# Performance work log

Measured on AMD Instinct MI355X. Metric: run time of the kernel, lower is better.

The kernel has to match this reference:

```python
import jax, jax.numpy as jnp
import numpy as np

N_X, N_UNITS, N_Y, N_U = 64, 256, 32, 64
BATCH = 32768


def setup_inputs() -> dict:
    key = jax.random.key(0)
    ks = jax.random.split(key, 10)
    nz = 2 * N_X + N_UNITS
    return {
        "u": jax.random.normal(ks[0], (BATCH, N_U, 1), dtype=jnp.float32),
        "x0": jax.random.normal(ks[1], (BATCH, N_X, 1), dtype=jnp.float32),
        # learned parameters (scaled down so H stays well-conditioned and tanh unsaturated)
        "B_2": 0.1 * jax.random.normal(ks[2], (N_X, N_U), dtype=jnp.float32),
        "C_2": 0.1 * jax.random.normal(ks[3], (N_Y, N_X), dtype=jnp.float32),
        "D_12": 0.1 * jax.random.normal(ks[4], (N_UNITS, N_U), dtype=jnp.float32),
        "D_21": 0.1 * jax.random.normal(ks[5], (N_Y, N_UNITS), dtype=jnp.float32),
        "b": 0.1 * jax.random.normal(ks[6], (N_X + N_UNITS + N_Y, 1), dtype=jnp.float32),
        "X": (1.0 / np.sqrt(nz)) * jax.random.normal(ks[7], (nz, nz), dtype=jnp.float32),
        "Y1": 0.1 * jax.random.normal(ks[8], (N_X, N_X), dtype=jnp.float32),
        # fixed IQC multipliers (train_qsr=False): Q nsd, R=I so Rinv=I; S stored transposed
        "S_t": 0.1 * jax.random.normal(ks[9], (N_U, N_Y), dtype=jnp.float32),
        "Q": -jnp.eye(N_Y, dtype=jnp.float32),
        "Rinv": jnp.eye(N_U, dtype=jnp.float32),
    }


def _constrained_weights(B_2, C_2, D_12, D_21, X, S_t, Q, Rinv):
    """Port of REN.updateConstrainedWeights (train_qsr=False). Returns C_1, D_11, lam."""
    n_x, n_units = B_2.shape[0], D_12.shape[0]
    n_y = C_2.shape[0]
    nz = 2 * n_x + n_units
    C2_ = S_t @ C_2                       # [n_u, n_x]
    D21_ = S_t @ D_21 - D_12.T            # [n_u, n_units]
    H = X.T @ X + 1e-3 * jnp.eye(nz, dtype=X.dtype)
    lT1 = jnp.concatenate([C2_.T, D21_.T, B_2], axis=0)          # [nz, n_u]
    H = H + lT1 @ Rinv @ lT1.T
    lT2 = jnp.concatenate([C_2.T, D_21.T, jnp.zeros((n_x, n_y), dtype=X.dtype)], axis=0)
    H = H - lT2 @ Q @ lT2.T
    H_21 = H[n_x:n_x + n_units, :n_x]
    H_22 = H[n_x:n_x + n_units, n_x:n_x + n_units]
    C_1 = -H_21                           # [n_units, n_x]
    lam = 0.5 * jnp.diag(H_22)            # Lambda diagonal, > 0 since H is PD
    # L = tril(-(H_22 - diag(H_22))) == -strictly_lower(H_22)
    D_11 = -jnp.tril(H_22, k=-1)          # strictly lower triangular [n_units, n_units]
    return C_1, D_11, lam


def _forward(u, x0, B_2, C_2, D_12, D_21, b, X, Y1, S_t, Q, Rinv):
    n_x, n_units = B_2.shape[0], D_12.shape[0]
    C_1, D_11, lam = _constrained_weights(B_2, C_2, D_12, D_21, X, S_t, Q, Rinv)
    u2 = u[:, :, 0]                       # [B, n_u]
    x2 = x0[:, :, 0]                      # [B, n_x]
    b_w = b[n_x:n_x + n_units, 0]         # [n_units]
    b_y = b[n_x + n_units:, 0]            # [n_y]
    # precompute the non-recurrent part of the pre-activation for all units
    v = x2 @ C_1.T + u2 @ D_12.T + b_w    # [B, n_units]
    # NOTE: the source uses D_11 row (i_unit - 1), not i_unit (faithful to original code).
    # For i=0 the source uses term2 = 0; D_11 is strictly lower so the full-row dot
    # against the partially-filled w (zeros beyond index i) matches D_11[i-1, :i] @ w[:i].
    Drows = jnp.concatenate([jnp.zeros((1, n_units), dtype=D_11.dtype), D_11[:-1]], axis=0)
    batch = u2.shape[0]

    def step(w, i):
        wi = jnp.tanh((v[:, i] + w @ Drows[i]) / lam[i])   # [B]
        w = w.at[:, i].set(wi)
        return w, None

    w0 = jnp.zeros((batch, n_units), dtype=v.dtype)
    w, _ = jax.lax.scan(step, w0, jnp.arange(n_units))
    y = x2 @ C_2.T + w @ D_21.T + b_y     # [B, n_y]
    return y[:, :, None]                  # [B, n_y, 1]


def reference(u, x0, B_2, C_2, D_12, D_21, b, X, Y1, S_t, Q, Rinv):
    return _forward(u, x0, B_2, C_2, D_12, D_21, b, X, Y1, S_t, Q, Rinv)
```

## Files before the change

### kernel.cpp

```cpp
#include <hip/hip_runtime.h>
#include <hip/hip_bf16.h>

typedef __attribute__((ext_vector_type(8))) short short8;
typedef __attribute__((ext_vector_type(4))) float floatx4;
typedef __attribute__((ext_vector_type(2))) float floatx2;

#define MFMA16 __builtin_amdgcn_mfma_f32_16x16x32_bf16

__device__ inline unsigned short bf16_rn(float f) {
    return (unsigned short)((__float_as_uint(f) + 0x8000u) >> 16);
}
__device__ __attribute__((always_inline)) inline short8 pack8v(float4 a, float4 b) {
    union { short8 s; unsigned int u[4]; } r;
    union { __hip_bfloat162 h; unsigned int u; } c;
    c.h = __float22bfloat162_rn(make_float2(a.x, a.y)); r.u[0] = c.u;
    c.h = __float22bfloat162_rn(make_float2(a.z, a.w)); r.u[1] = c.u;
    c.h = __float22bfloat162_rn(make_float2(b.x, b.y)); r.u[2] = c.u;
    c.h = __float22bfloat162_rn(make_float2(b.z, b.w)); r.u[3] = c.u;
    return r.s;
}

__global__ __launch_bounds__(64) void ren_prep13(
    const float* __restrict__ B2, const float* __restrict__ C2,
    const float* __restrict__ D12, const float* __restrict__ D21,
    const float* __restrict__ St, const float* __restrict__ Q,
    const float* __restrict__ Rinv,
    float* __restrict__ lT1, float* __restrict__ t1,
    float* __restrict__ lT2, float* __restrict__ t2,
    unsigned short* __restrict__ Wvb, unsigned short* __restrict__ C2b,
    unsigned short* __restrict__ D21b)
{
    const int t = threadIdx.x;
    const int blk = blockIdx.x;
    if (blk >= 384) {
        const int id = (blk - 384) * 64 + t;
        if (id < 16384) {
            Wvb[(id >> 6) * 128 + 64 + (id & 63)] = bf16_rn(D12[id]);
        } else if (id < 16384 + 2048) {
            C2b[id - 16384] = bf16_rn(C2[id - 16384]);
        } else if (id < 16384 + 2048 + 8192) {
            D21b[id - 18432] = bf16_rn(D21[id - 18432]);
        }
        return;
    }

    __shared__ float stl[64 * 33];
    __shared__ float colbuf[32];
    __shared__ float s1[64];

    const int r = blk;
    const int c = t;
#pragma unroll
    for (int j = 0; j < 32; j++) {
        const int id = j * 64 + t;
        stl[(id >> 5) * 33 + (id & 31)] = St[id];
    }
    if (t < 32)
        colbuf[t] = (r < 64) ? C2[t * 64 + r]
                  : (r < 320 ? D21[t * 256 + (r - 64)] : 0.f);
    __syncthreads();

    float v1;
    if (r < 64) {
        float s = 0.f;
#pragma unroll
        for (int p = 0; p < 32; p++) s += stl[c * 33 + p] * colbuf[p];
        v1 = s;
    } else if (r < 320) {
        float s = 0.f;
#pragma unroll
        for (int p = 0; p < 32; p++) s += stl[c * 33 + p] * colbuf[p];
        v1 = s - D12[(r - 64) * 64 + c];
    } else {
        v1 = B2[(r - 320) * 64 + c];
    }
    s1[c] = v1;
    lT1[r * 64 + c] = v1;
    if (c < 32) {
        const float v2 = (r < 320) ? colbuf[c] : 0.f;
        lT2[r * 32 + c] = v2;
    }
    __syncthreads();

    float a = 0.f;
#pragma unroll
    for (int k = 0; k < 64; k++) a += s1[k] * Rinv[k * 64 + c];
    t1[r * 64 + c] = a;

    if (c < 32) {
        float bq = 0.f;
#pragma unroll
        for (int k = 0; k < 32; k++) bq += colbuf[k] * Q[k * 32 + c];
        t2[r * 32 + c] = bq;
    }
}

__global__ __launch_bounds__(320) void ren_prep2(
    const float* __restrict__ X,
    const float* __restrict__ lT1, const float* __restrict__ t1,
    const float* __restrict__ lT2, const float* __restrict__ t2,
    unsigned short* __restrict__ Wvb, unsigned short* __restrict__ Drowsb,
    float* __restrict__ Dpair, float* __restrict__ lamg)
{
    __shared__ float xcol[384];
    const int c = threadIdx.x;
    const int i = blockIdx.x;
    for (int t = c; t < 384; t += 320) xcol[t] = X[t * 384 + 64 + i];
    __syncthreads();

    float f0 = 0.f, f1 = 0.f, f2 = 0.f, f3 = 0.f;
    float ac[8], au[8], bc8[8], bu[8];
#pragma unroll
    for (int kk = 0; kk < 8; kk++) { ac[kk] = X[kk * 384 + c]; au[kk] = xcol[kk]; }
    for (int k0 = 0; k0 < 384; k0 += 16) {
#pragma unroll
        for (int kk = 0; kk < 8; kk++) {
            bc8[kk] = X[(k0 + 8 + kk) * 384 + c]; bu[kk] = xcol[k0 + 8 + kk];
        }
        f0 += au[0] * ac[0]; f1 += au[1] * ac[1];
        f2 += au[2] * ac[2]; f3 += au[3] * ac[3];
        f0 += au[4] * ac[4]; f1 += au[5] * ac[5];
        f2 += au[6] * ac[6]; f3 += au[7] * ac[7];
        if (k0 + 16 < 384) {
#pragma unroll
            for (int kk = 0; kk < 8; kk++) {
                ac[kk] = X[(k0 + 16 + kk) * 384 + c]; au[kk] = xcol[k0 + 16 + kk];
            }
        }
        f0 += bu[0] * bc8[0]; f1 += bu[1] * bc8[1];
        f2 += bu[2] * bc8[2]; f3 += bu[3] * bc8[3];
        f0 += bu[4] * bc8[4]; f1 += bu[5] * bc8[5];
        f2 += bu[6] * bc8[6]; f3 += bu[7] * bc8[7];
    }

    const float* __restrict__ t1r = t1 + (64 + i) * 64;
    const float* __restrict__ l1r = lT1 + c * 64;
#pragma unroll
    for (int m4 = 0; m4 < 16; m4++) {
        const float4 lv = *(const float4*)(l1r + m4 * 4);
        f0 += t1r[m4 * 4 + 0] * lv.x; f1 += t1r[m4 * 4 + 1] * lv.y;
        f2 += t1r[m4 * 4 + 2] * lv.z; f3 += t1r[m4 * 4 + 3] * lv.w;
    }
    const float* __restrict__ t2r = t2 + (64 + i) * 32;
    const float* __restrict__ l2r = lT2 + c * 32;
#pragma unroll
    for (int m4 = 0; m4 < 8; m4++) {
        const float4 lv = *(const float4*)(l2r + m4 * 4);
        f0 -= t2r[m4 * 4 + 0] * lv.x; f1 -= t2r[m4 * 4 + 1] * lv.y;
        f2 -= t2r[m4 * 4 + 2] * lv.z; f3 -= t2r[m4 * 4 + 3] * lv.w;
    }
    float acc = (f0 + f1) + (f2 + f3) + (((64 + i) == c) ? 0.001f : 0.f);

    if (c < 64) {
        Wvb[i * 128 + c] = bf16_rn(-acc);
    } else {
        const int cb = c - 64;
        if (cb == i) lamg[i] = 5.7707801635558536f / acc;
        if (i < 255) {
            const float dv = (cb <= i - 1) ? -acc : 0.f;
            Drowsb[(i + 1) * 256 + cb] = bf16_rn(dv);
            const int row = i + 1;
            if ((row >> 4) == (cb >> 4)) {
                const int q = row & 15, p = cb & 15;
                Dpair[(row >> 4) * 256 + (q >> 1) * 32 + p * 2 + (q & 1)] = dv;
            }
        } else {
            Drowsb[cb] = 0;
        }
    }
}

__device__ __attribute__((always_inline)) inline void triangle16x2(
    float (&vlA)[16], float (&wlA)[16],
    float (&vlB)[16], float (&wlB)[16],
    const float* __restrict__ dblk, const float* __restrict__ lam)
{
#pragma unroll
    for (int tq = 0; tq < 8; tq++) {
        floatx2 aA, bA, aB, bB;
        aA[0] = vlA[2 * tq]; aA[1] = vlA[2 * tq + 1];
        aB[0] = vlB[2 * tq]; aB[1] = vlB[2 * tq + 1];
        bA[0] = 0.f; bA[1] = 0.f;
        bB[0] = 0.f; bB[1] = 0.f;
#pragma unroll
        for (int p4 = 0; p4 < tq; p4++) {
            const float4 d4 = *(const float4*)&dblk[tq * 32 + p4 * 4];
            floatx2 de; de[0] = d4.x; de[1] = d4.y;
            floatx2 dz; dz[0] = d4.z; dz[1] = d4.w;
            aA += de * wlA[2 * p4];  bA += dz * wlA[2 * p4 + 1];
            aB += de * wlB[2 * p4];  bB += dz * wlB[2 * p4 + 1];
        }
        aA += bA; aB += bB;
        floatx2 lm2; lm2[0] = lam[2 * tq]; lm2[1] = lam[2 * tq + 1];
        aA *= lm2; aB *= lm2;
        const float e0A = __builtin_amdgcn_exp2f(aA[0]);
        const float e1A = __builtin_amdgcn_exp2f(aA[1]);
        const float e0B = __builtin_amdgcn_exp2f(aB[0]);
        const float e1B = __builtin_amdgcn_exp2f(aB[1]);
        wlA[2 * tq]     = 1.f - 2.f * __builtin_amdgcn_rcpf(e0A + 1.f);
        wlA[2 * tq + 1] = 1.f - 2.f * __builtin_amdgcn_rcpf(e1A + 1.f);
        wlB[2 * tq]     = 1.f - 2.f * __builtin_amdgcn_rcpf(e0B + 1.f);
        wlB[2 * tq + 1] = 1.f - 2.f * __builtin_amdgcn_rcpf(e1B + 1.f);
    }
}

__global__ __launch_bounds__(64, 1) void ren_main(
    const float* __restrict__ u, const float* __restrict__ x0,
    const float* __restrict__ b,
    const unsigned short* __restrict__ Wvb,
    const unsigned short* __restrict__ Drowsb,
    const float* __restrict__ Dpair,
    const float* __restrict__ lamg,
    const unsigned short* __restrict__ C2b,
    const unsigned short* __restrict__ D21b,
    float* __restrict__ out)
{
    __shared__ float bufA[16][20];
    __shared__ float bufB[16][20];
    __shared__ float dblk[256];
    __shared__ float lamsh[256];
    __shared__ float bsh[256];
    __shared__ short8 wshA[8 * 64];
    __shared__ short8 wshB[8 * 64];

    const int L = threadIdx.x;
    const int col = L & 15;
    const int quad = L >> 4;
    const int row0 = blockIdx.x * 32;

#pragma unroll
    for (int j = 0; j < 4; j++) {
        lamsh[j * 64 + L] = lamg[j * 64 + L];
        bsh[j * 64 + L]   = b[64 + j * 64 + L];
    }
    const short8 zero8 = {0, 0, 0, 0, 0, 0, 0, 0};
#pragma unroll
    for (int c = 0; c < 8; c++) { wshA[c * 64 + L] = zero8; wshB[c * 64 + L] = zero8; }

    short8 zfA[4], zfB[4];
#pragma unroll
    for (int c = 0; c < 4; c++) {
        const float* base = (c < 2 ? x0 : u);
        const float* pA = base + (long)(row0 + col) * 64 + (c & 1) * 32 + quad * 8;
        const float* pB = base + (long)(row0 + 16 + col) * 64 + (c & 1) * 32 + quad * 8;
        zfA[c] = pack8v(*(const float4*)pA, *(const float4*)(pA + 4));
        zfB[c] = pack8v(*(const float4*)pB, *(const float4*)(pB + 4));
    }

    float4 dcur = *(const float4*)(Dpair + 4 * L);
    floatx4 accA0 = {0.f, 0.f, 0.f, 0.f}, accA1 = {0.f, 0.f, 0.f, 0.f};
    floatx4 accB0 = {0.f, 0.f, 0.f, 0.f}, accB1 = {0.f, 0.f, 0.f, 0.f};
    {
        short8 v0 = *(const short8*)(Wvb + col * 128 + quad * 8);
        short8 v1 = *(const short8*)(Wvb + col * 128 + 32 + quad * 8);
        short8 v2 = *(const short8*)(Wvb + col * 128 + 64 + quad * 8);
        short8 v3 = *(const short8*)(Wvb + col * 128 + 96 + quad * 8);
        accA0 = MFMA16(zfA[0], v0, accA0, 0, 0, 0);
        accB0 = MFMA16(zfB[0], v0, accB0, 0, 0, 0);
        accA1 = MFMA16(zfA[1], v1, accA1, 0, 0, 0);
        accB1 = MFMA16(zfB[1], v1, accB1, 0, 0, 0);
        accA0 = MFMA16(zfA[2], v2, accA0, 0, 0, 0);
        accB0 = MFMA16(zfB[2], v2, accB0, 0, 0, 0);
        accA1 = MFMA16(zfA[3], v3, accA1, 0, 0, 0);
        accB1 = MFMA16(zfB[3], v3, accB1, 0, 0, 0);
    }

#pragma unroll 1
    for (int n = 0; n < 15; n++) {
        const int rb = 16 * (n + 1) + col;
        float4 dnxt = *(const float4*)(Dpair + (n + 1) * 256 + 4 * L);
        short8 vf[4];
#pragma unroll
        for (int c = 0; c < 4; c++)
            vf[c] = *(const short8*)(Wvb + rb * 128 + c * 32 + quad * 8);

        *(float4*)&dblk[4 * L] = dcur;
        const float bwv = bsh[16 * n + col];
#pragma unroll
        for (int r = 0; r < 4; r++) {
            bufA[quad * 4 + r][col] = accA0[r] + accA1[r] + bwv;
            bufB[quad * 4 + r][col] = accB0[r] + accB1[r] + bwv;
        }

        float vlA[16], wlA[16], vlB[16], wlB[16];
#pragma unroll
        for (int p4 = 0; p4 < 4; p4++) {
            const float4 ta = *(const float4*)&bufA[col][p4 * 4];
            const float4 tb = *(const float4*)&bufB[col][p4 * 4];
            vlA[p4 * 4 + 0] = ta.x; vlA[p4 * 4 + 1] = ta.y;
            vlA[p4 * 4 + 2] = ta.z; vlA[p4 * 4 + 3] = ta.w;
            vlB[p4 * 4 + 0] = tb.x; vlB[p4 * 4 + 1] = tb.y;
            vlB[p4 * 4 + 2] = tb.z; vlB[p4 * 4 + 3] = tb.w;
        }

        triangle16x2(vlA, wlA, vlB, wlB, dblk, &lamsh[16 * n]);

        {
            float4 waA, wbA, waB, wbB;
            if (quad & 1) {
                waA = make_float4(wlA[8], wlA[9], wlA[10], wlA[11]);
                wbA = make_float4(wlA[12], wlA[13], wlA[14], wlA[15]);
                waB = make_float4(wlB[8], wlB[9], wlB[10], wlB[11]);
                wbB = make_float4(wlB[12], wlB[13], wlB[14], wlB[15]);
            } else {
                waA = make_float4(wlA[0], wlA[1], wlA[2], wlA[3]);
                wbA = make_float4(wlA[4], wlA[5], wlA[6], wlA[7]);
                waB = make_float4(wlB[0], wlB[1], wlB[2], wlB[3]);
                wbB = make_float4(wlB[4], wlB[5], wlB[6], wlB[7]);
            }
            const short8 nfA = pack8v(waA, wbA);
            const short8 nfB = pack8v(waB, wbB);
            if ((quad >> 1) == (n & 1)) {
                wshA[(n >> 1) * 64 + L] = nfA;
                wshB[(n >> 1) * 64 + L] = nfB;
            }
        }

        floatx4 aA0 = {0.f, 0.f, 0.f, 0.f}, aA1 = {0.f, 0.f, 0.f, 0.f};
        floatx4 aB0 = {0.f, 0.f, 0.f, 0.f}, aB1 = {0.f, 0.f, 0.f, 0.f};
        aA0 = MFMA16(zfA[0], vf[0], aA0, 0, 0, 0);
        aB0 = MFMA16(zfB[0], vf[0], aB0, 0, 0, 0);
        aA1 = MFMA16(zfA[1], vf[1], aA1, 0, 0, 0);
        aB1 = MFMA16(zfB[1], vf[1], aB1, 0, 0, 0);
        aA0 = MFMA16(zfA[2], vf[2], aA0, 0, 0, 0);
        aB0 = MFMA16(zfB[2], vf[2], aB0, 0, 0, 0);
        aA1 = MFMA16(zfA[3], vf[3], aA1, 0, 0, 0);
        aB1 = MFMA16(zfB[3], vf[3], aB1, 0, 0, 0);
        const int lim = (n + 2) >> 1;
#pragma unroll 1
        for (int c = 0; c < lim; c++) {
            const short8 h = *(const short8*)(Drowsb + rb * 256 + c * 32 + quad * 8);
            const short8 wA = wshA[c * 64 + L];
            const short8 wB = wshB[c * 64 + L];
            if (c & 1) {
                aA1 = MFMA16(wA, h, aA1, 0, 0, 0);
                aB1 = MFMA16(wB, h, aB1, 0, 0, 0);
            } else {
                aA0 = MFMA16(wA, h, aA0, 0, 0, 0);
                aB0 = MFMA16(wB, h, aB0, 0, 0, 0);
            }
        }
        accA0 = aA0; accA1 = aA1; accB0 = aB0; accB1 = aB1;
        dcur = dnxt;
    }

    {
        *(float4*)&dblk[4 * L] = dcur;
        const float bwv = bsh[240 + col];
#pragma unroll
        for (int r = 0; r < 4; r++) {
            bufA[quad * 4 + r][col] = accA0[r] + accA1[r] + bwv;
            bufB[quad * 4 + r][col] = accB0[r] + accB1[r] + bwv;
        }

        float vlA[16], wlA[16], vlB[16], wlB[16];
#pragma unroll
        for (int p4 = 0; p4 < 4; p4++) {
            const float4 ta = *(const float4*)&bufA[col][p4 * 4];
            const float4 tb = *(const float4*)&bufB[col][p4 * 4];
            vlA[p4 * 4 + 0] = ta.x; vlA[p4 * 4 + 1] = ta.y;
            vlA[p4 * 4 + 2] = ta.z; vlA[p4 * 4 + 3] = ta.w;
            vlB[p4 * 4 + 0] = tb.x; vlB[p4 * 4 + 1] = tb.y;
            vlB[p4 * 4 + 2] = tb.z; vlB[p4 * 4 + 3] = tb.w;
        }

        triangle16x2(vlA, wlA, vlB, wlB, dblk, &lamsh[240]);

        float4 waA, wbA, waB, wbB;
        if (quad & 1) {
            waA = make_float4(wlA[8], wlA[9], wlA[10], wlA[11]);
            wbA = make_float4(wlA[12], wlA[13], wlA[14], wlA[15]);
            waB = make_float4(wlB[8], wlB[9], wlB[10], wlB[11]);
            wbB = make_float4(wlB[12], wlB[13], wlB[14], wlB[15]);
        } else {
            waA = make_float4(wlA[0], wlA[1], wlA[2], wlA[3]);
            wbA = make_float4(wlA[4], wlA[5], wlA[6], wlA[7]);
            waB = make_float4(wlB[0], wlB[1], wlB[2], wlB[3]);
            wbB = make_float4(wlB[4], wlB[5], wlB[6], wlB[7]);
        }
        const short8 nfA = pack8v(waA, wbA);
        const short8 nfB = pack8v(waB, wbB);
        if (quad >= 2) {
            wshA[7 * 64 + L] = nfA;
            wshB[7 * 64 + L] = nfB;
        }
    }

    floatx4 yA0 = {0.f, 0.f, 0.f, 0.f}, yA1 = {0.f, 0.f, 0.f, 0.f};
    floatx4 yB0 = {0.f, 0.f, 0.f, 0.f}, yB1 = {0.f, 0.f, 0.f, 0.f};
    {
        const short8 yc0 = *(const short8*)(C2b + col * 64 + quad * 8);
        const short8 yc1 = *(const short8*)(C2b + col * 64 + 32 + quad * 8);
        const short8 yc2 = *(const short8*)(C2b + (16 + col) * 64 + quad * 8);
        const short8 yc3 = *(const short8*)(C2b + (16 + col) * 64 + 32 + quad * 8);
        yA0 = MFMA16(zfA[0], yc0, yA0, 0, 0, 0);
        yB0 = MFMA16(zfB[0], yc0, yB0, 0, 0, 0);
        yA1 = MFMA16(zfA[0], yc2, yA1, 0, 0, 0);
        yB1 = MFMA16(zfB[0], yc2, yB1, 0, 0, 0);
        yA0 = MFMA16(zfA[1], yc1, yA0, 0, 0, 0);
        yB0 = MFMA16(zfB[1], yc1, yB0, 0, 0, 0);
        yA1 = MFMA16(zfA[1], yc3, yA1, 0, 0, 0);
        yB1 = MFMA16(zfB[1], yc3, yB1, 0, 0, 0);
    }
#pragma unroll
    for (int c = 0; c < 8; c++) {
        const short8 wA = wshA[c * 64 + L];
        const short8 wB = wshB[c * 64 + L];
        const short8 b0 = *(const short8*)(D21b + col * 256 + c * 32 + quad * 8);
        const short8 b1 = *(const short8*)(D21b + (16 + col) * 256 + c * 32 + quad * 8);
        yA0 = MFMA16(wA, b0, yA0, 0, 0, 0);
        yB0 = MFMA16(wB, b0, yB0, 0, 0, 0);
        yA1 = MFMA16(wA, b1, yA1, 0, 0, 0);
        yB1 = MFMA16(wB, b1, yB1, 0, 0, 0);
    }
    const float by0 = b[320 + col];
    const float by1 = b[336 + col];
#pragma unroll
    for (int r = 0; r < 4; r++) {
        out[(long)(row0 + quad * 4 + r) * 32 + col]           = yA0[r] + by0;
        out[(long)(row0 + quad * 4 + r) * 32 + 16 + col]      = yA1[r] + by1;
        out[(long)(row0 + 16 + quad * 4 + r) * 32 + col]      = yB0[r] + by0;
        out[(long)(row0 + 16 + quad * 4 + r) * 32 + 16 + col] = yB1[r] + by1;
    }
}

extern "C" void kernel_launch(void* const* d_in, const int* in_sizes, int n_in,
                              void* d_out, int out_size, void* d_ws, size_t ws_size,
                              hipStream_t stream)
{
    const float* u    = (const float*)d_in[0];
    const float* x0   = (const float*)d_in[1];
    const float* B2   = (const float*)d_in[2];
    const float* C2   = (const float*)d_in[3];
    const float* D12  = (const float*)d_in[4];
    const float* D21  = (const float*)d_in[5];
    const float* b    = (const float*)d_in[6];
    const float* X    = (const float*)d_in[7];
    const float* St   = (const float*)d_in[9];
    const float* Q    = (const float*)d_in[10];
    const float* Rinv = (const float*)d_in[11];
    float* out = (float*)d_out;

    float* ws     = (float*)d_ws;
    float* lT1    = ws;
    float* t1     = lT1 + 384 * 64;
    float* lT2    = t1 + 384 * 64;
    float* t2     = lT2 + 384 * 32;
    float* lamg   = t2 + 384 * 32;
    float* Dpair  = lamg + 256;
    unsigned short* Drowsb = (unsigned short*)(Dpair + 16 * 256);
    unsigned short* Wvb    = Drowsb + 256 * 256;
    unsigned short* C2b    = Wvb + 256 * 128;
    unsigned short* D21b   = C2b + 32 * 64;

    ren_prep13<<<dim3(800), dim3(64), 0, stream>>>(B2, C2, D12, D21, St, Q, Rinv,
                                                   lT1, t1, lT2, t2, Wvb, C2b, D21b);
    ren_prep2<<<dim3(256), dim3(320), 0, stream>>>(X, lT1, t1, lT2, t2,
                                                   Wvb, Drowsb, Dpair, lamg);

    const int batch = in_sizes[0] / 64;
    ren_main<<<dim3(batch / 32), dim3(64), 0, stream>>>(u, x0, b, Wvb, Drowsb,
                                                        Dpair, lamg, C2b, D21b, out);
}
```

Measured before the change: 137.6 us.

## Prefetch next block's weights into double-buffered registers and fully unroll Drows loop

Restructures the 15-step recurrent block loop into unrolled pairs. Each step now preloads the Wvb and Drows fragments for the following block into register buffers that alternate between steps, so the global loads overlap the triangle solve and MFMAs. The inner Drows loop becomes a fixed, fully unrolled 8-chunk loop. This removes the loop control and the load-use stalls, but it always runs 8 chunks of MFMAs even where only a few are needed. It also raises register pressure and relies on the not-yet-written shared w chunks multiplying zero weights harmlessly.

```diff
diff --git a/kernel.cpp b/kernel.cpp
--- a/kernel.cpp
+++ b/kernel.cpp
@@ -204,6 +204,78 @@
     }
 }
 
+#define REN_ITER(n_, VC, HC, VN, HN, DO_LOAD_)                                 \
+  {                                                                            \
+    const int nI = (n_);                                                       \
+    if (DO_LOAD_) {                                                            \
+      const int rb2 = 16 * (nI + 2) + col;                                     \
+      _Pragma("unroll") for (int cc = 0; cc < 4; cc++)                         \
+        VN[cc] = *(const short8*)(Wvb + rb2 * 128 + cc * 32 + quad * 8);       \
+      _Pragma("unroll") for (int cc = 0; cc < 8; cc++)                         \
+        HN[cc] = *(const short8*)(Drowsb + rb2 * 256 + cc * 32 + quad * 8);    \
+    }                                                                          \
+    const float4 dnxtI = *(const float4*)(Dpair + (nI + 1) * 256 + 4 * L);     \
+    *(float4*)&dblk[4 * L] = dcur;                                             \
+    const float bwvI = bsh[16 * nI + col];                                     \
+    _Pragma("unroll") for (int r = 0; r < 4; r++) {                            \
+      bufA[quad * 4 + r][col] = accA0[r] + accA1[r] + bwvI;                    \
+      bufB[quad * 4 + r][col] = accB0[r] + accB1[r] + bwvI;                    \
+    }                                                                          \
+    float vlA[16], wlA[16], vlB[16], wlB[16];                                  \
+    _Pragma("unroll") for (int p4 = 0; p4 < 4; p4++) {                         \
+      const float4 ta = *(const float4*)&bufA[col][p4 * 4];                    \
+      const float4 tb = *(const float4*)&bufB[col][p4 * 4];                    \
+      vlA[p4 * 4 + 0] = ta.x; vlA[p4 * 4 + 1] = ta.y;                          \
+      vlA[p4 * 4 + 2] = ta.z; vlA[p4 * 4 + 3] = ta.w;                          \
+      vlB[p4 * 4 + 0] = tb.x; vlB[p4 * 4 + 1] = tb.y;                          \
+      vlB[p4 * 4 + 2] = tb.z; vlB[p4 * 4 + 3] = tb.w;                          \
+    }                                                                          \
+    triangle16x2(vlA, wlA, vlB, wlB, dblk, &lamsh[16 * nI]);                   \
+    {                                                                          \
+      float4 waA, wbA, waB, wbB;                                               \
+      if (quad & 1) {                                                          \
+        waA = make_float4(wlA[8], wlA[9], wlA[10], wlA[11]);                   \
+        wbA = make_float4(wlA[12], wlA[13], wlA[14], wlA[15]);                 \
+        waB = make_float4(wlB[8], wlB[9], wlB[10], wlB[11]);                   \
+        wbB = make_float4(wlB[12], wlB[13], wlB[14], wlB[15]);                 \
+      } else {                                                                 \
+        waA = make_float4(wlA[0], wlA[1], wlA[2], wlA[3]);                     \
+        wbA = make_float4(wlA[4], wlA[5], wlA[6], wlA[7]);                     \
+        waB = make_float4(wlB[0], wlB[1], wlB[2], wlB[3]);                     \
+        wbB = make_float4(wlB[4], wlB[5], wlB[6], wlB[7]);                     \
+      }                                                                        \
+      const short8 nfA = pack8v(waA, wbA);                                     \
+      const short8 nfB = pack8v(waB, wbB);                                     \
+      if ((quad >> 1) == (nI & 1)) {                                           \
+        wshA[(nI >> 1) * 64 + L] = nfA;                                        \
+        wshB[(nI >> 1) * 64 + L] = nfB;                                        \
+      }                                                                        \
+    }                                                                          \
+    floatx4 aA0 = {0.f, 0.f, 0.f, 0.f}, aA1 = {0.f, 0.f, 0.f, 0.f};            \
+    floatx4 aB0 = {0.f, 0.f, 0.f, 0.f}, aB1 = {0.f, 0.f, 0.f, 0.f};            \
+    aA0 = MFMA16(zfA[0], VC[0], aA0, 0, 0, 0);                                 \
+    aB0 = MFMA16(zfB[0], VC[0], aB0, 0, 0, 0);                                 \
+    aA1 = MFMA16(zfA[1], VC[1], aA1, 0, 0, 0);                                 \
+    aB1 = MFMA16(zfB[1], VC[1], aB1, 0, 0, 0);                                 \
+    aA0 = MFMA16(zfA[2], VC[2], aA0, 0, 0, 0);                                 \
+    aB0 = MFMA16(zfB[2], VC[2], aB0, 0, 0, 0);                                 \
+    aA1 = MFMA16(zfA[3], VC[3], aA1, 0, 0, 0);                                 \
+    aB1 = MFMA16(zfB[3], VC[3], aB1, 0, 0, 0);                                 \
+    _Pragma("unroll") for (int cc = 0; cc < 8; cc++) {                         \
+      const short8 wA = wshA[cc * 64 + L];                                     \
+      const short8 wB = wshB[cc * 64 + L];                                     \
+      if (cc & 1) {                                                            \
+        aA1 = MFMA16(wA, HC[cc], aA1, 0, 0, 0);                                \
+        aB1 = MFMA16(wB, HC[cc], aB1, 0, 0, 0);                                \
+      } else {                                                                 \
+        aA0 = MFMA16(wA, HC[cc], aA0, 0, 0, 0);                                \
+        aB0 = MFMA16(wB, HC[cc], aB0, 0, 0, 0);                                \
+      }                                                                        \
+    }                                                                          \
+    accA0 = aA0; accA1 = aA1; accB0 = aB0; accB1 = aB1;                        \
+    dcur = dnxtI;                                                              \
+  }
+
 __global__ __launch_bounds__(64, 1) void ren_main(
     const float* __restrict__ u, const float* __restrict__ x0,
     const float* __restrict__ b,
@@ -265,84 +337,23 @@
         accB1 = MFMA16(zfB[3], v3, accB1, 0, 0, 0);
     }
 
+    short8 sv0[4], sh0[8], sv1[4], sh1[8];
+    {
+        const int rb = 16 + col;
+#pragma unroll
+        for (int c = 0; c < 4; c++)
+            sv1[c] = *(const short8*)(Wvb + rb * 128 + c * 32 + quad * 8);
+#pragma unroll
+        for (int c = 0; c < 8; c++)
+            sh1[c] = *(const short8*)(Drowsb + rb * 256 + c * 32 + quad * 8);
+    }
+
 #pragma unroll 1
-    for (int n = 0; n < 15; n++) {
-        const int rb = 16 * (n + 1) + col;
-        float4 dnxt = *(const float4*)(Dpair + (n + 1) * 256 + 4 * L);
-        short8 vf[4];
-#pragma unroll
-        for (int c = 0; c < 4; c++)
-            vf[c] = *(const short8*)(Wvb + rb * 128 + c * 32 + quad * 8);
-
-        *(float4*)&dblk[4 * L] = dcur;
-        const float bwv = bsh[16 * n + col];
-#pragma unroll
-        for (int r = 0; r < 4; r++) {
-            bufA[quad * 4 + r][col] = accA0[r] + accA1[r] + bwv;
-            bufB[quad * 4 + r][col] = accB0[r] + accB1[r] + bwv;
-        }
-
-        float vlA[16], wlA[16], vlB[16], wlB[16];
-#pragma unroll
-        for (int p4 = 0; p4 < 4; p4++) {
-            const float4 ta = *(const float4*)&bufA[col][p4 * 4];
-            const float4 tb = *(const float4*)&bufB[col][p4 * 4];
-            vlA[p4 * 4 + 0] = ta.x; vlA[p4 * 4 + 1] = ta.y;
-            vlA[p4 * 4 + 2] = ta.z; vlA[p4 * 4 + 3] = ta.w;
-            vlB[p4 * 4 + 0] = tb.x; vlB[p4 * 4 + 1] = tb.y;
-            vlB[p4 * 4 + 2] = tb.z; vlB[p4 * 4 + 3] = tb.w;
-        }
-
-        triangle16x2(vlA, wlA, vlB, wlB, dblk, &lamsh[16 * n]);
-
-        {
-            float4 waA, wbA, waB, wbB;
-            if (quad & 1) {
-                waA = make_float4(wlA[8], wlA[9], wlA[10], wlA[11]);
-                wbA = make_float4(wlA[12], wlA[13], wlA[14], wlA[15]);
-                waB = make_float4(wlB[8], wlB[9], wlB[10], wlB[11]);
-                wbB = make_float4(wlB[12], wlB[13], wlB[14], wlB[15]);
-            } else {
-                waA = make_float4(wlA[0], wlA[1], wlA[2], wlA[3]);
-                wbA = make_float4(wlA[4], wlA[5], wlA[6], wlA[7]);
-                waB = make_float4(wlB[0], wlB[1], wlB[2], wlB[3]);
-                wbB = make_float4(wlB[4], wlB[5], wlB[6], wlB[7]);
-            }
-            const short8 nfA = pack8v(waA, wbA);
-            const short8 nfB = pack8v(waB, wbB);
-            if ((quad >> 1) == (n & 1)) {
-                wshA[(n >> 1) * 64 + L] = nfA;
-                wshB[(n >> 1) * 64 + L] = nfB;
-            }
-        }
-
-        floatx4 aA0 = {0.f, 0.f, 0.f, 0.f}, aA1 = {0.f, 0.f, 0.f, 0.f};
-        floatx4 aB0 = {0.f, 0.f, 0.f, 0.f}, aB1 = {0.f, 0.f, 0.f, 0.f};
-        aA0 = MFMA16(zfA[0], vf[0], aA0, 0, 0, 0);
-        aB0 = MFMA16(zfB[0], vf[0], aB0, 0, 0, 0);
-        aA1 = MFMA16(zfA[1], vf[1], aA1, 0, 0, 0);
-        aB1 = MFMA16(zfB[1], vf[1], aB1, 0, 0, 0);
-        aA0 = MFMA16(zfA[2], vf[2], aA0, 0, 0, 0);
-        aB0 = MFMA16(zfB[2], vf[2], aB0, 0, 0, 0);
-        aA1 = MFMA16(zfA[3], vf[3], aA1, 0, 0, 0);
-        aB1 = MFMA16(zfB[3], vf[3], aB1, 0, 0, 0);
-        const int lim = (n + 2) >> 1;
-#pragma unroll 1
-        for (int c = 0; c < lim; c++) {
-            const short8 h = *(const short8*)(Drowsb + rb * 256 + c * 32 + quad * 8);
-            const short8 wA = wshA[c * 64 + L];
-            const short8 wB = wshB[c * 64 + L];
-            if (c & 1) {
-                aA1 = MFMA16(wA, h, aA1, 0, 0, 0);
-                aB1 = MFMA16(wB, h, aB1, 0, 0, 0);
-            } else {
-                aA0 = MFMA16(wA, h, aA0, 0, 0, 0);
-                aB0 = MFMA16(wB, h, aB0, 0, 0, 0);
-            }
-        }
-        accA0 = aA0; accA1 = aA1; accB0 = aB0; accB1 = aB1;
-        dcur = dnxt;
-    }
+    for (int np = 0; np < 7; np++) {
+        REN_ITER(2 * np,     sv1, sh1, sv0, sh0, 1)
+        REN_ITER(2 * np + 1, sv0, sh0, sv1, sh1, 1)
+    }
+    REN_ITER(14, sv1, sh1, sv0, sh0, 0)
 
     {
         *(float4*)&dblk[4 * L] = dcur;
```

Measured after the change: 126.1 us. 1.09x faster.
